# Kernel optimization log

Measured on AMD Instinct MI355X. Metric: run time of the kernel, lower is better.

Reference implementation:

```python
import jax, jax.numpy as jnp
import numpy as np

COMMITMENT_COST = 0.25


def setup_inputs() -> dict:
    key = jax.random.key(0)
    k1, k2 = jax.random.split(key)
    cnt_emb = jax.random.normal(k1, (64, 2048, 80), dtype=jnp.float32)
    embed_weight = jax.random.normal(k2, (1024, 80), dtype=jnp.float32)  # nn.Embedding(n_embed, n_mel).weight
    return {"cnt_emb": cnt_emb, "embed_weight": embed_weight}


def reference(cnt_emb, embed_weight):
    # embed: detached, transposed [n_mel, n_embed], column-normalized (only for distance computation)
    embed = jax.lax.stop_gradient(embed_weight).T  # [80, 1024]
    embed = embed / jnp.linalg.norm(embed, axis=0, keepdims=True)

    flatten = jax.lax.stop_gradient(cnt_emb.reshape(-1, cnt_emb.shape[-1]))  # [N, 80]
    dist = (
        jnp.sum(flatten * flatten, axis=1, keepdims=True)
        - 2.0 * (flatten @ embed)
        + jnp.sum(embed * embed, axis=0, keepdims=True)
    )  # [N, n_embed]
    embed_ind = jnp.argmax(-dist, axis=1).reshape(cnt_emb.shape[:-1])  # [B, T]

    # gather from the UNnormalized embedding table (as nn.Embedding lookup)
    quantized = embed_weight[embed_ind]  # [B, T, 80]

    e_latent_loss = jnp.mean((jax.lax.stop_gradient(quantized) - cnt_emb) ** 2)
    q_latent_loss = jnp.mean((quantized - jax.lax.stop_gradient(cnt_emb)) ** 2)
    loss = q_latent_loss + COMMITMENT_COST * e_latent_loss

    # straight-through estimator
    quantized = cnt_emb + jax.lax.stop_gradient(quantized - cnt_emb)
    return quantized, loss
```

## Files before the change

kernel.cpp:

```cpp
#include <hip/hip_runtime.h>

#define D   80
#define NE  1024
#define HS  128
#define NH  (NE / HS)
#define CAP 32
#define MARGIN 0.5f

#define OFF_ACC  0
#define OFF_EN   64
#define OFF_EC   327744
#define OFF_ENBT 331840
#define OFF_CNT  1019968
#define OFF_LIST 1544256
#define WS_NEED  9932864

typedef __attribute__((ext_vector_type(8))) short  bf16x8;
typedef __attribute__((ext_vector_type(4))) float  f32x4;

static __device__ __forceinline__ short f2bf(float f) {
    unsigned u = __float_as_uint(f);
    return (short)((u + 0x7fffu + ((u >> 16) & 1u)) >> 16);
}

static __device__ __forceinline__ bf16x8 cvt8(const float* p) {
    float4 f0 = *(const float4*)p;
    float4 f1 = *(const float4*)(p + 4);
    bf16x8 a;
    a[0] = f2bf(f0.x); a[1] = f2bf(f0.y); a[2] = f2bf(f0.z); a[3] = f2bf(f0.w);
    a[4] = f2bf(f1.x); a[5] = f2bf(f1.y); a[6] = f2bf(f1.z); a[7] = f2bf(f1.w);
    return a;
}

static __device__ __forceinline__ void gload_lds16(const void* g, void* l) {
    __builtin_amdgcn_global_load_lds(
        (const __attribute__((address_space(1))) unsigned int*)g,
        (__attribute__((address_space(3))) unsigned int*)l, 16, 0, 0);
}

__global__ __launch_bounds__(256) void vq_prep(const float* __restrict__ w,
                                               float* __restrict__ en,
                                               float* __restrict__ ec,
                                               char* __restrict__ enbT) {
    int j = blockIdx.x * blockDim.x + threadIdx.x;
    if (j >= NE) return;
    const float* wj = w + j * D;
    float s = __fmul_rn(wj[0], wj[0]);
    for (int k = 1; k < D; ++k) s = __fadd_rn(s, __fmul_rn(wj[k], wj[k]));
    float norm = __fsqrt_rn(s);
    float* ej = en + j * D;
    float c = 0.f;
    for (int k = 0; k < D; ++k) {
        float v = __fdiv_rn(wj[k], norm);
        ej[k] = v;
        float sq = __fmul_rn(v, v);
        c = (k == 0) ? sq : __fadd_rn(c, sq);
    }
    ec[j] = c;
    for (int cc = 0; cc < 10; ++cc) {
        bf16x8 b;
#pragma unroll
        for (int e = 0; e < 8; ++e)
            b[e] = f2bf(__fmul_rn(-2.0f, ej[cc * 8 + e]));
        *(bf16x8*)(enbT + cc * 16384 + j * 16) = b;
    }
}

__global__ __launch_bounds__(256)
__attribute__((amdgpu_waves_per_eu(4, 4)))
void vq_mfma(
        const float* __restrict__ x,
        const char* __restrict__ enbT,
        int* __restrict__ cnt,
        unsigned short* __restrict__ list,
        int n) {
    __shared__ __align__(16) char lds[2][20480];

    const int tid  = threadIdx.x;
    const int lane = tid & 63;
    const int wv   = tid >> 6;
    const int row0 = blockIdx.x * 128 + wv * 32;
    const int l15  = lane & 15;
    const int lg   = lane >> 4;

    bf16x8 A0[2], A1[2], A2[2];
#pragma unroll
    for (int rt = 0; rt < 2; ++rt) {
        const float* xr = x + (size_t)(row0 + rt * 16 + l15) * D;
        A0[rt] = cvt8(xr + lg * 8);
        A1[rt] = cvt8(xr + 32 + lg * 8);
        if (lg < 2) A2[rt] = cvt8(xr + 64 + lg * 8);
        else { bf16x8 z = {}; A2[rt] = z; }
    }

#define STAGE(b, h) do {                                                      \
        _Pragma("unroll")                                                     \
        for (int t = 0; t < 5; ++t) {                                         \
            int slot = tid + t * 256;                                         \
            gload_lds16(enbT + (size_t)(slot >> 7) * 16384 + (h) * 2048       \
                             + (slot & 127) * 16,                             \
                        &lds[b][0] + slot * 16);                              \
        }                                                                     \
    } while (0)

    float vmin[2][4];
#pragma unroll
    for (int rt = 0; rt < 2; ++rt)
#pragma unroll
        for (int r = 0; r < 4; ++r) vmin[rt][r] = 3.4e38f;

    STAGE(0, 0);
    for (int h = 0; h < NH; ++h) {
        __syncthreads();
        if (h + 1 < NH) STAGE((h + 1) & 1, h + 1);
        const char* buf = &lds[h & 1][0];
        for (int e16 = 0; e16 < 8; ++e16) {
            const char* base = buf + (e16 * 16 + l15) * 16;
            bf16x8 B0 = *(const bf16x8*)(base + lg * 2048);
            bf16x8 B1 = *(const bf16x8*)(base + (4 + lg) * 2048);
            bf16x8 B2 = *(const bf16x8*)(base + (8 + (lg & 1)) * 2048);
#pragma unroll
            for (int rt = 0; rt < 2; ++rt) {
                f32x4 c = {0.f, 0.f, 0.f, 0.f};
                c = __builtin_amdgcn_mfma_f32_16x16x32_bf16(A0[rt], B0, c, 0, 0, 0);
                c = __builtin_amdgcn_mfma_f32_16x16x32_bf16(A1[rt], B1, c, 0, 0, 0);
                c = __builtin_amdgcn_mfma_f32_16x16x32_bf16(A2[rt], B2, c, 0, 0, 0);
#pragma unroll
                for (int r = 0; r < 4; ++r) vmin[rt][r] = fminf(vmin[rt][r], c[r]);
            }
        }
    }

    float thr[2][4];
#pragma unroll
    for (int rt = 0; rt < 2; ++rt)
#pragma unroll
        for (int r = 0; r < 4; ++r) {
            float v = vmin[rt][r];
#pragma unroll
            for (int m = 1; m < 16; m <<= 1) v = fminf(v, __shfl_xor(v, m));
            thr[rt][r] = v + MARGIN;
        }

    STAGE(0, 0);
    for (int h = 0; h < NH; ++h) {
        __syncthreads();
        if (h + 1 < NH) STAGE((h + 1) & 1, h + 1);
        const char* buf = &lds[h & 1][0];
        for (int e16 = 0; e16 < 8; ++e16) {
            const char* base = buf + (e16 * 16 + l15) * 16;
            bf16x8 B0 = *(const bf16x8*)(base + lg * 2048);
            bf16x8 B1 = *(const bf16x8*)(base + (4 + lg) * 2048);
            bf16x8 B2 = *(const bf16x8*)(base + (8 + (lg & 1)) * 2048);
            int jj = h * HS + e16 * 16 + l15;
#pragma unroll
            for (int rt = 0; rt < 2; ++rt) {
                f32x4 c = {0.f, 0.f, 0.f, 0.f};
                c = __builtin_amdgcn_mfma_f32_16x16x32_bf16(A0[rt], B0, c, 0, 0, 0);
                c = __builtin_amdgcn_mfma_f32_16x16x32_bf16(A1[rt], B1, c, 0, 0, 0);
                c = __builtin_amdgcn_mfma_f32_16x16x32_bf16(A2[rt], B2, c, 0, 0, 0);
                bool h0 = c[0] <= thr[rt][0], h1 = c[1] <= thr[rt][1];
                bool h2 = c[2] <= thr[rt][2], h3 = c[3] <= thr[rt][3];
                if (__any(h0 | h1 | h2 | h3)) {
#pragma unroll
                    for (int r = 0; r < 4; ++r) {
                        bool hh = (r == 0) ? h0 : (r == 1) ? h1 : (r == 2) ? h2 : h3;
                        if (hh) {
                            int row = row0 + rt * 16 + lg * 4 + r;
                            int o = atomicAdd(cnt + row, 1);
                            if (o < CAP)
                                list[(size_t)row * CAP + o] = (unsigned short)jj;
                        }
                    }
                }
            }
        }
    }
#undef STAGE
}

__global__ __launch_bounds__(256)
__attribute__((amdgpu_waves_per_eu(1, 2)))
void vq_exact_epi(const float* __restrict__ x,
                  const float* __restrict__ en,
                  const float* __restrict__ ec,
                  const int* __restrict__ cnt,
                  const unsigned short* __restrict__ list,
                  const float* __restrict__ w,
                  float* __restrict__ out,
                  double* __restrict__ loss_acc, int n) {
    __shared__ int sbidx[256];
    __shared__ double bsum[4];
    const int row = blockIdx.x * 256 + threadIdx.x;

    int bi = 0;
    if (row < n) {
        int c = cnt[row];
        float X[D];
        const float4* x4 = (const float4*)(x + (size_t)row * D);
#pragma unroll
        for (int i = 0; i < D / 4; ++i) {
            float4 v = x4[i];
            X[4 * i + 0] = v.x; X[4 * i + 1] = v.y;
            X[4 * i + 2] = v.z; X[4 * i + 3] = v.w;
        }
        float pr[8];
#pragma unroll
        for (int t = 0; t < 8; ++t) pr[t] = __fmul_rn(X[t], X[t]);
#pragma unroll
        for (int base = 8; base < D; base += 8)
#pragma unroll
            for (int t = 0; t < 8; ++t)
                pr[t] = __fadd_rn(pr[t], __fmul_rn(X[base + t], X[base + t]));
        float A = __fadd_rn(
            __fadd_rn(__fadd_rn(pr[0], pr[1]), __fadd_rn(pr[2], pr[3])),
            __fadd_rn(__fadd_rn(pr[4], pr[5]), __fadd_rn(pr[6], pr[7])));

        float best = 3.4e38f;
        bi = -1;
        if (c > 0 && c <= CAP) {
            for (int i = 0; i < c; ++i) {
                int j = list[(size_t)row * CAP + i];
                const float* ej = en + j * D;
                float d = 0.f;
#pragma unroll
                for (int k = 0; k < D; ++k) d = __builtin_fmaf(X[k], ej[k], d);
                float s = __fadd_rn(__fsub_rn(A, __fmul_rn(2.0f, d)), ec[j]);
                if (s < best || (s == best && j < bi)) { best = s; bi = j; }
            }
        } else {
            for (int j = 0; j < NE; ++j) {
                const float* ej = en + j * D;
                float d = 0.f;
#pragma unroll
                for (int k = 0; k < D; ++k) d = __builtin_fmaf(X[k], ej[k], d);
                float s = __fadd_rn(__fsub_rn(A, __fmul_rn(2.0f, d)), ec[j]);
                if (s < best) { best = s; bi = j; }
            }
        }
    }
    sbidx[threadIdx.x] = bi;
    __syncthreads();

    const int row0 = blockIdx.x * 256;
    double ss = 0.0;
#pragma unroll
    for (int t = 0; t < 20; ++t) {
        int f  = threadIdx.x + t * 256;
        int rr = f / 20;
        int k4 = (f % 20) * 4;
        int gr = row0 + rr;
        if (gr < n) {
            int gbi = sbidx[rr];
            float4 q  = *(const float4*)(w + gbi * D + k4);
            float4 xv = *(const float4*)(x + (size_t)gr * D + k4);
            float d0 = __fsub_rn(q.x, xv.x), d1 = __fsub_rn(q.y, xv.y);
            float d2 = __fsub_rn(q.z, xv.z), d3 = __fsub_rn(q.w, xv.w);
            float4 o;
            o.x = __fadd_rn(xv.x, d0); o.y = __fadd_rn(xv.y, d1);
            o.z = __fadd_rn(xv.z, d2); o.w = __fadd_rn(xv.w, d3);
            *(float4*)(out + (size_t)gr * D + k4) = o;
            ss += (double)__fmul_rn(d0, d0) + (double)__fmul_rn(d1, d1);
            ss += (double)__fmul_rn(d2, d2) + (double)__fmul_rn(d3, d3);
        }
    }
#pragma unroll
    for (int off = 32; off > 0; off >>= 1) ss += __shfl_down(ss, off);
    int wid = threadIdx.x >> 6;
    if ((threadIdx.x & 63) == 0) bsum[wid] = ss;
    __syncthreads();
    if (threadIdx.x == 0)
        atomicAdd(loss_acc, bsum[0] + bsum[1] + bsum[2] + bsum[3]);
}

__global__ void vq_fin_kernel(const double* __restrict__ acc,
                              float* __restrict__ out_loss,
                              double count) {
    float m = (float)(*acc / count);
    *out_loss = __fadd_rn(m, __fmul_rn(0.25f, m));
}

__global__ __launch_bounds__(64)
__attribute__((amdgpu_waves_per_eu(2, 2)))
void vq_main_exact(const float* __restrict__ x, const float* __restrict__ w,
                   const float* __restrict__ en, const float* __restrict__ ec,
                   float* __restrict__ out, double* __restrict__ loss_acc, int n) {
    const int r = blockIdx.x * 64 + threadIdx.x;
    double ss = 0.0;
    if (r < n) {
        float X[D];
        const float4* x4 = (const float4*)(x + (size_t)r * D);
#pragma unroll
        for (int i = 0; i < D / 4; ++i) {
            float4 v = x4[i];
            X[4 * i + 0] = v.x; X[4 * i + 1] = v.y;
            X[4 * i + 2] = v.z; X[4 * i + 3] = v.w;
        }
        float pr[8];
#pragma unroll
        for (int t = 0; t < 8; ++t) pr[t] = __fmul_rn(X[t], X[t]);
#pragma unroll
        for (int base = 8; base < D; base += 8)
#pragma unroll
            for (int t = 0; t < 8; ++t)
                pr[t] = __fadd_rn(pr[t], __fmul_rn(X[base + t], X[base + t]));
        float A = __fadd_rn(
            __fadd_rn(__fadd_rn(pr[0], pr[1]), __fadd_rn(pr[2], pr[3])),
            __fadd_rn(__fadd_rn(pr[4], pr[5]), __fadd_rn(pr[6], pr[7])));
        float best = 3.4e38f; int bi = 0;
        for (int j = 0; j < NE; ++j) {
            const float* ej = en + j * D;
            float d = 0.f;
#pragma unroll
            for (int k = 0; k < D; ++k) d = __builtin_fmaf(X[k], ej[k], d);
            float s = __fadd_rn(__fsub_rn(A, __fmul_rn(2.0f, d)), ec[j]);
            if (s < best) { best = s; bi = j; }
        }
        const float* wj = w + bi * D;
        float4* o4 = (float4*)(out + (size_t)r * D);
#pragma unroll
        for (int i = 0; i < D / 4; ++i) {
            float q0 = wj[4*i+0], q1 = wj[4*i+1], q2 = wj[4*i+2], q3 = wj[4*i+3];
            float d0 = __fsub_rn(q0, X[4*i+0]), d1 = __fsub_rn(q1, X[4*i+1]);
            float d2 = __fsub_rn(q2, X[4*i+2]), d3 = __fsub_rn(q3, X[4*i+3]);
            float4 o;
            o.x = __fadd_rn(X[4*i+0], d0); o.y = __fadd_rn(X[4*i+1], d1);
            o.z = __fadd_rn(X[4*i+2], d2); o.w = __fadd_rn(X[4*i+3], d3);
            o4[i] = o;
            ss += (double)__fmul_rn(d0, d0) + (double)__fmul_rn(d1, d1);
            ss += (double)__fmul_rn(d2, d2) + (double)__fmul_rn(d3, d3);
        }
    }
#pragma unroll
    for (int off = 32; off > 0; off >>= 1) ss += __shfl_down(ss, off);
    if (threadIdx.x == 0) atomicAdd(loss_acc, ss);
}

extern "C" void kernel_launch(void* const* d_in, const int* in_sizes, int n_in,
                              void* d_out, int out_size, void* d_ws, size_t ws_size,
                              hipStream_t stream) {
    const float* x = (const float*)d_in[0];
    const float* w = (const float*)d_in[1];
    float* out = (float*)d_out;
    int n = in_sizes[0] / D;

    char* ws = (char*)d_ws;
    double* acc = (double*)(ws + OFF_ACC);
    float*  en  = (float*)(ws + OFF_EN);
    float*  ec  = (float*)(ws + OFF_EC);

    hipMemsetAsync(ws + OFF_ACC, 0, 64, stream);
    if (ws_size >= WS_NEED) {
        char*  enbT = ws + OFF_ENBT;
        int*   cnt  = (int*)(ws + OFF_CNT);
        unsigned short* list = (unsigned short*)(ws + OFF_LIST);
        hipMemsetAsync(cnt, 0, (size_t)n * 4, stream);
        vq_prep<<<(NE + 255) / 256, 256, 0, stream>>>(w, en, ec, enbT);
        vq_mfma<<<n / 128, 256, 0, stream>>>(x, enbT, cnt, list, n);
        vq_exact_epi<<<(n + 255) / 256, 256, 0, stream>>>(x, en, ec, cnt, list,
                                                          w, out, acc, n);
    } else {
        char* enbT_dummy = ws + OFF_EC + 4096;
        vq_prep<<<(NE + 255) / 256, 256, 0, stream>>>(w, en, ec, enbT_dummy);
        vq_main_exact<<<(n + 63) / 64, 64, 0, stream>>>(x, w, en, ec, out, acc, n);
    }
    vq_fin_kernel<<<1, 1, 0, stream>>>(acc, out + (size_t)n * D, (double)n * D);
}
```

Baseline: 159.1 us.

## Replace two-pass MFMA candidate scan with single-pass per-lane top-3 tracking

The MFMA kernel now keeps a per-lane top-3 of approximate distances in one pass over the codebook instead of doing a min pass followed by a second thresholded collection pass. Rows whose third-best candidate is still within the margin are flagged and resolved by a new cleanup kernel that does a block-parallel exact scan. Rows with a single candidate then skip the fp32 rescoring in the epilogue. This removes half the MFMA work and the per-hit atomics, at the cost of extra register pressure for top-3 state and an additional kernel launch.

```diff
diff --git a/kernel.cpp b/kernel.cpp
--- a/kernel.cpp
+++ b/kernel.cpp
@@ -5,6 +5,7 @@
 #define HS  128
 #define NH  (NE / HS)
 #define CAP 32
+#define FLAGBIT 0x40000000
 #define MARGIN 0.5f
 
 #define OFF_ACC  0
@@ -103,11 +104,15 @@
         }                                                                     \
     } while (0)
 
-    float vmin[2][4];
+    float m1[2][4], m2[2][4], m3[2][4];
+    int   j1[2][4], j2[2][4];
 #pragma unroll
     for (int rt = 0; rt < 2; ++rt)
 #pragma unroll
-        for (int r = 0; r < 4; ++r) vmin[rt][r] = 3.4e38f;
+        for (int r = 0; r < 4; ++r) {
+            m1[rt][r] = 3.4e38f; m2[rt][r] = 3.4e38f; m3[rt][r] = 3.4e38f;
+            j1[rt][r] = 0; j2[rt][r] = 0;
+        }
 
     STAGE(0, 0);
     for (int h = 0; h < NH; ++h) {
@@ -119,6 +124,7 @@
             bf16x8 B0 = *(const bf16x8*)(base + lg * 2048);
             bf16x8 B1 = *(const bf16x8*)(base + (4 + lg) * 2048);
             bf16x8 B2 = *(const bf16x8*)(base + (8 + (lg & 1)) * 2048);
+            const int jj = h * HS + e16 * 16 + l15;
 #pragma unroll
             for (int rt = 0; rt < 2; ++rt) {
                 f32x4 c = {0.f, 0.f, 0.f, 0.f};
@@ -126,57 +132,131 @@
                 c = __builtin_amdgcn_mfma_f32_16x16x32_bf16(A1[rt], B1, c, 0, 0, 0);
                 c = __builtin_amdgcn_mfma_f32_16x16x32_bf16(A2[rt], B2, c, 0, 0, 0);
 #pragma unroll
-                for (int r = 0; r < 4; ++r) vmin[rt][r] = fminf(vmin[rt][r], c[r]);
-            }
-        }
-    }
-
-    float thr[2][4];
-#pragma unroll
-    for (int rt = 0; rt < 2; ++rt)
-#pragma unroll
-        for (int r = 0; r < 4; ++r) {
-            float v = vmin[rt][r];
-#pragma unroll
-            for (int m = 1; m < 16; m <<= 1) v = fminf(v, __shfl_xor(v, m));
-            thr[rt][r] = v + MARGIN;
-        }
-
-    STAGE(0, 0);
-    for (int h = 0; h < NH; ++h) {
-        __syncthreads();
-        if (h + 1 < NH) STAGE((h + 1) & 1, h + 1);
-        const char* buf = &lds[h & 1][0];
-        for (int e16 = 0; e16 < 8; ++e16) {
-            const char* base = buf + (e16 * 16 + l15) * 16;
-            bf16x8 B0 = *(const bf16x8*)(base + lg * 2048);
-            bf16x8 B1 = *(const bf16x8*)(base + (4 + lg) * 2048);
-            bf16x8 B2 = *(const bf16x8*)(base + (8 + (lg & 1)) * 2048);
-            int jj = h * HS + e16 * 16 + l15;
-#pragma unroll
-            for (int rt = 0; rt < 2; ++rt) {
-                f32x4 c = {0.f, 0.f, 0.f, 0.f};
-                c = __builtin_amdgcn_mfma_f32_16x16x32_bf16(A0[rt], B0, c, 0, 0, 0);
-                c = __builtin_amdgcn_mfma_f32_16x16x32_bf16(A1[rt], B1, c, 0, 0, 0);
-                c = __builtin_amdgcn_mfma_f32_16x16x32_bf16(A2[rt], B2, c, 0, 0, 0);
-                bool h0 = c[0] <= thr[rt][0], h1 = c[1] <= thr[rt][1];
-                bool h2 = c[2] <= thr[rt][2], h3 = c[3] <= thr[rt][3];
-                if (__any(h0 | h1 | h2 | h3)) {
-#pragma unroll
-                    for (int r = 0; r < 4; ++r) {
-                        bool hh = (r == 0) ? h0 : (r == 1) ? h1 : (r == 2) ? h2 : h3;
-                        if (hh) {
-                            int row = row0 + rt * 16 + lg * 4 + r;
-                            int o = atomicAdd(cnt + row, 1);
-                            if (o < CAP)
-                                list[(size_t)row * CAP + o] = (unsigned short)jj;
+                for (int r = 0; r < 4; ++r) {
+                    float cv = c[r];
+                    if (cv < m3[rt][r]) {
+                        bool lt2 = cv < m2[rt][r];
+                        bool lt1 = cv < m1[rt][r];
+                        m3[rt][r] = lt2 ? m2[rt][r] : cv;
+                        if (lt2) {
+                            if (lt1) {
+                                m2[rt][r] = m1[rt][r]; j2[rt][r] = j1[rt][r];
+                                m1[rt][r] = cv;        j1[rt][r] = jj;
+                            } else {
+                                m2[rt][r] = cv;        j2[rt][r] = jj;
+                            }
                         }
                     }
                 }
             }
         }
     }
+
+#pragma unroll
+    for (int rt = 0; rt < 2; ++rt)
+#pragma unroll
+        for (int r = 0; r < 4; ++r) {
+            float v = m1[rt][r];
+#pragma unroll
+            for (int m = 1; m < 16; m <<= 1) v = fminf(v, __shfl_xor(v, m));
+            float t_ = v + MARGIN;
+            int fl = (m3[rt][r] <= t_) ? 1 : 0;
+#pragma unroll
+            for (int m = 1; m < 16; m <<= 1) fl |= __shfl_xor(fl, m);
+            int row = row0 + rt * 16 + lg * 4 + r;
+            if (fl) {
+                if (l15 == 0) atomicOr(cnt + row, FLAGBIT);
+            } else {
+                bool c1 = m1[rt][r] <= t_;
+                bool c2 = m2[rt][r] <= t_;
+                if (c1) {
+                    int o = atomicAdd(cnt + row, 1);
+                    if (o < CAP)
+                        list[(size_t)row * CAP + o] = (unsigned short)j1[rt][r];
+                }
+                if (c2) {
+                    int o = atomicAdd(cnt + row, 1);
+                    if (o < CAP)
+                        list[(size_t)row * CAP + o] = (unsigned short)j2[rt][r];
+                }
+            }
+        }
 #undef STAGE
+}
+
+__global__ __launch_bounds__(256)
+__attribute__((amdgpu_waves_per_eu(1, 2)))
+void vq_cleanup(const float* __restrict__ x,
+                const float* __restrict__ en,
+                const float* __restrict__ ec,
+                int* __restrict__ cnt,
+                unsigned short* __restrict__ list, int n) {
+    __shared__ int frows[128];
+    __shared__ int nf;
+    __shared__ float sS[4];
+    __shared__ int   sJ[4];
+    const int tid = threadIdx.x;
+    if (tid == 0) nf = 0;
+    __syncthreads();
+    int r0 = blockIdx.x * 128;
+    if (tid < 128) {
+        int row = r0 + tid;
+        if (row < n && (cnt[row] & FLAGBIT)) {
+            int i = atomicAdd(&nf, 1);
+            frows[i] = row;
+        }
+    }
+    __syncthreads();
+    const int nfl = nf;
+    for (int i = 0; i < nfl; ++i) {
+        const int row = frows[i];
+        float X[D];
+        const float4* x4 = (const float4*)(x + (size_t)row * D);
+#pragma unroll
+        for (int q = 0; q < D / 4; ++q) {
+            float4 v = x4[q];
+            X[4 * q + 0] = v.x; X[4 * q + 1] = v.y;
+            X[4 * q + 2] = v.z; X[4 * q + 3] = v.w;
+        }
+        float pr[8];
+#pragma unroll
+        for (int t = 0; t < 8; ++t) pr[t] = __fmul_rn(X[t], X[t]);
+#pragma unroll
+        for (int base = 8; base < D; base += 8)
+#pragma unroll
+            for (int t = 0; t < 8; ++t)
+                pr[t] = __fadd_rn(pr[t], __fmul_rn(X[base + t], X[base + t]));
+        float A = __fadd_rn(
+            __fadd_rn(__fadd_rn(pr[0], pr[1]), __fadd_rn(pr[2], pr[3])),
+            __fadd_rn(__fadd_rn(pr[4], pr[5]), __fadd_rn(pr[6], pr[7])));
+
+        float best = 3.4e38f; int bj = NE;
+        for (int j = tid; j < NE; j += 256) {
+            const float* ej = en + j * D;
+            float d = 0.f;
+#pragma unroll
+            for (int k = 0; k < D; ++k) d = __builtin_fmaf(X[k], ej[k], d);
+            float s = __fadd_rn(__fsub_rn(A, __fmul_rn(2.0f, d)), ec[j]);
+            if (s < best || (s == best && j < bj)) { best = s; bj = j; }
+        }
+#pragma unroll
+        for (int off = 32; off > 0; off >>= 1) {
+            float ob = __shfl_down(best, off);
+            int   oj = __shfl_down(bj, off);
+            if (ob < best || (ob == best && oj < bj)) { best = ob; bj = oj; }
+        }
+        if ((tid & 63) == 0) { sS[tid >> 6] = best; sJ[tid >> 6] = bj; }
+        __syncthreads();
+        if (tid == 0) {
+            float b = sS[0]; int j = sJ[0];
+#pragma unroll
+            for (int w2 = 1; w2 < 4; ++w2)
+                if (sS[w2] < b || (sS[w2] == b && sJ[w2] < j)) { b = sS[w2]; j = sJ[w2]; }
+            list[(size_t)row * CAP] = (unsigned short)j;
+            cnt[row] = 1;
+        }
+        __syncthreads();
+    }
 }
 
 __global__ __launch_bounds__(256)
@@ -196,46 +276,50 @@
     int bi = 0;
     if (row < n) {
         int c = cnt[row];
-        float X[D];
-        const float4* x4 = (const float4*)(x + (size_t)row * D);
-#pragma unroll
-        for (int i = 0; i < D / 4; ++i) {
-            float4 v = x4[i];
-            X[4 * i + 0] = v.x; X[4 * i + 1] = v.y;
-            X[4 * i + 2] = v.z; X[4 * i + 3] = v.w;
-        }
-        float pr[8];
-#pragma unroll
-        for (int t = 0; t < 8; ++t) pr[t] = __fmul_rn(X[t], X[t]);
-#pragma unroll
-        for (int base = 8; base < D; base += 8)
-#pragma unroll
-            for (int t = 0; t < 8; ++t)
-                pr[t] = __fadd_rn(pr[t], __fmul_rn(X[base + t], X[base + t]));
-        float A = __fadd_rn(
-            __fadd_rn(__fadd_rn(pr[0], pr[1]), __fadd_rn(pr[2], pr[3])),
-            __fadd_rn(__fadd_rn(pr[4], pr[5]), __fadd_rn(pr[6], pr[7])));
-
-        float best = 3.4e38f;
-        bi = -1;
-        if (c > 0 && c <= CAP) {
-            for (int i = 0; i < c; ++i) {
-                int j = list[(size_t)row * CAP + i];
-                const float* ej = en + j * D;
-                float d = 0.f;
-#pragma unroll
-                for (int k = 0; k < D; ++k) d = __builtin_fmaf(X[k], ej[k], d);
-                float s = __fadd_rn(__fsub_rn(A, __fmul_rn(2.0f, d)), ec[j]);
-                if (s < best || (s == best && j < bi)) { best = s; bi = j; }
+        if (c == 1) {
+            bi = list[(size_t)row * CAP];
+        } else {
+            float X[D];
+            const float4* x4 = (const float4*)(x + (size_t)row * D);
+#pragma unroll
+            for (int i = 0; i < D / 4; ++i) {
+                float4 v = x4[i];
+                X[4 * i + 0] = v.x; X[4 * i + 1] = v.y;
+                X[4 * i + 2] = v.z; X[4 * i + 3] = v.w;
             }
-        } else {
-            for (int j = 0; j < NE; ++j) {
-                const float* ej = en + j * D;
-                float d = 0.f;
-#pragma unroll
-                for (int k = 0; k < D; ++k) d = __builtin_fmaf(X[k], ej[k], d);
-                float s = __fadd_rn(__fsub_rn(A, __fmul_rn(2.0f, d)), ec[j]);
-                if (s < best) { best = s; bi = j; }
+            float pr[8];
+#pragma unroll
+            for (int t = 0; t < 8; ++t) pr[t] = __fmul_rn(X[t], X[t]);
+#pragma unroll
+            for (int base = 8; base < D; base += 8)
+#pragma unroll
+                for (int t = 0; t < 8; ++t)
+                    pr[t] = __fadd_rn(pr[t], __fmul_rn(X[base + t], X[base + t]));
+            float A = __fadd_rn(
+                __fadd_rn(__fadd_rn(pr[0], pr[1]), __fadd_rn(pr[2], pr[3])),
+                __fadd_rn(__fadd_rn(pr[4], pr[5]), __fadd_rn(pr[6], pr[7])));
+
+            float best = 3.4e38f;
+            bi = -1;
+            if (c >= 2 && c <= CAP) {
+                for (int i = 0; i < c; ++i) {
+                    int j = list[(size_t)row * CAP + i];
+                    const float* ej = en + j * D;
+                    float d = 0.f;
+#pragma unroll
+                    for (int k = 0; k < D; ++k) d = __builtin_fmaf(X[k], ej[k], d);
+                    float s = __fadd_rn(__fsub_rn(A, __fmul_rn(2.0f, d)), ec[j]);
+                    if (s < best || (s == best && j < bi)) { best = s; bi = j; }
+                }
+            } else {
+                for (int j = 0; j < NE; ++j) {
+                    const float* ej = en + j * D;
+                    float d = 0.f;
+#pragma unroll
+                    for (int k = 0; k < D; ++k) d = __builtin_fmaf(X[k], ej[k], d);
+                    float s = __fadd_rn(__fsub_rn(A, __fmul_rn(2.0f, d)), ec[j]);
+                    if (s < best) { best = s; bi = j; }
+                }
             }
         }
     }
@@ -357,6 +441,7 @@
         hipMemsetAsync(cnt, 0, (size_t)n * 4, stream);
         vq_prep<<<(NE + 255) / 256, 256, 0, stream>>>(w, en, ec, enbT);
         vq_mfma<<<n / 128, 256, 0, stream>>>(x, enbT, cnt, list, n);
+        vq_cleanup<<<(n + 127) / 128, 256, 0, stream>>>(x, en, ec, cnt, list, n);
         vq_exact_epi<<<(n + 255) / 256, 256, 0, stream>>>(x, en, ec, cnt, list,
                                                           w, out, acc, n);
     } else {
```

Result: slower. 191.4 us (+20.3%).
